# Kernel tuning notes

Hardware: AMD Instinct MI355X
Metric: run time of the kernel (lower is better)

The kernel has to match this reference:

```python
import jax, jax.numpy as jnp
import numpy as np

B, F, H = 16384, 2048, 4096   # batch, n_features, n_hidden
D, K = 4096, 2048             # num_of_demos, num_of_features


def setup_inputs() -> dict:
    key = jax.random.key(0)
    ks = jax.random.split(key, 16)
    s = 0.02
    return {
        "x": jax.random.normal(ks[0], (B, F), jnp.float32),
        "demo_metric": jax.random.uniform(ks[1], (D, K), jnp.float32),
        "alpha": jax.random.normal(ks[2], (K,), jnp.float32),
        "sample_loss": jax.random.uniform(ks[3], (D, K), jnp.float32),
        "subdom_constant": jax.random.uniform(ks[4], (1,), jnp.float32),
        "num_of_demos": D,
        "num_of_features": K,
        "W1": jax.random.normal(ks[5], (F, H), jnp.float32) * s,
        "b1": jnp.zeros((H,), jnp.float32),
        "W2": jax.random.normal(ks[6], (H, H), jnp.float32) * s,
        "b2": jnp.zeros((H,), jnp.float32),
        "W3": jax.random.normal(ks[7], (H, H), jnp.float32) * s,
        "b3": jnp.zeros((H,), jnp.float32),
        "W4": jax.random.normal(ks[8], (H, 2), jnp.float32) * s,
        "b4": jnp.zeros((2,), jnp.float32),
    }


def reference(x, demo_metric, alpha, sample_loss, subdom_constant,
              num_of_demos, num_of_features,
              W1, b1, W2, b2, W3, b3, W4, b4):
    # subdom hinge loss: max(alpha_k * (sample_loss_jk - demo_loss_jk) + 1, 0) - c
    margin = alpha[None, :] * (sample_loss - demo_metric) + 1.0  # [D, K]
    subdom = jnp.maximum(margin, 0.0) - subdom_constant          # broadcast c
    loss = jnp.sum(subdom)

    # MLP classifier (dropout = identity at inference) + sigmoid
    h = jax.nn.relu(x @ W1 + b1)
    h = jax.nn.relu(h @ W2 + b2)
    h = jax.nn.relu(h @ W3 + b3)
    probs = jax.nn.sigmoid(h @ W4 + b4)  # [B, 2]
    return (loss, probs)
```

## Files before the change

### kernel.cpp

```cpp
#include <hip/hip_runtime.h>
#include <cstdint>
#include <cstddef>

typedef unsigned short u16;
typedef __attribute__((ext_vector_type(8))) __bf16 bf16x8;
typedef __attribute__((ext_vector_type(4))) float f32x4;

__device__ __forceinline__ u16 f2bf(float f) {
  union { float f; unsigned u; } v; v.f = f;
  unsigned r = v.u + 0x7FFFu + ((v.u >> 16) & 1u);
  return (u16)(r >> 16);
}
__device__ __forceinline__ float bf2f(unsigned h) {
  union { unsigned u; float f; } v; v.u = h << 16;
  return v.f;
}

__global__ void init_loss_kernel(const float* __restrict__ c,
                                 const int* __restrict__ D,
                                 const int* __restrict__ K,
                                 float* __restrict__ out) {
  out[0] = -c[0] * (float)D[0] * (float)K[0];
}

__global__ void subdom_kernel(const float4* __restrict__ dm,
                              const float4* __restrict__ sl,
                              const float4* __restrict__ alpha4,
                              float* __restrict__ out, int n4, int k4mask) {
  const int stride = gridDim.x * blockDim.x;
  float s = 0.f;
  for (int i = blockIdx.x * blockDim.x + threadIdx.x; i < n4; i += stride) {
    float4 d = dm[i], l = sl[i], a = alpha4[i & k4mask];
    s += fmaxf(fmaf(a.x, l.x - d.x, 1.f), 0.f);
    s += fmaxf(fmaf(a.y, l.y - d.y, 1.f), 0.f);
    s += fmaxf(fmaf(a.z, l.z - d.z, 1.f), 0.f);
    s += fmaxf(fmaf(a.w, l.w - d.w, 1.f), 0.f);
  }
#pragma unroll
  for (int off = 32; off > 0; off >>= 1) s += __shfl_down(s, off, 64);
  __shared__ float red[4];
  const int lane = threadIdx.x & 63, wave = threadIdx.x >> 6;
  if (lane == 0) red[wave] = s;
  __syncthreads();
  if (threadIdx.x == 0) atomicAdd(out, red[0] + red[1] + red[2] + red[3]);
}

__global__ void cast_f32_bf16_kernel(const float4* __restrict__ in,
                                     u16* __restrict__ out, int n4) {
  const int stride = gridDim.x * blockDim.x;
  for (int i = blockIdx.x * blockDim.x + threadIdx.x; i < n4; i += stride) {
    float4 v = in[i];
    uint2 p;
    p.x = (unsigned)f2bf(v.x) | ((unsigned)f2bf(v.y) << 16);
    p.y = (unsigned)f2bf(v.z) | ((unsigned)f2bf(v.w) << 16);
    ((uint2*)out)[i] = p;
  }
}

__global__ void transpose_cast_kernel(const float* __restrict__ in,
                                      u16* __restrict__ out, int K, int N) {
  __shared__ float tile[32][33];
  const int bx = blockIdx.x * 32;
  const int by = blockIdx.y * 32;
  const int tx = threadIdx.x, ty = threadIdx.y;
#pragma unroll
  for (int i = ty; i < 32; i += 8)
    tile[i][tx] = in[(size_t)(by + i) * N + bx + tx];
  __syncthreads();
#pragma unroll
  for (int i = ty; i < 32; i += 8)
    out[(size_t)(bx + i) * K + by + tx] = f2bf(tile[tx][i]);
}


__device__ __forceinline__ void gload_lds16(const void* g, void* l) {
  __builtin_amdgcn_global_load_lds(
      (const __attribute__((address_space(1))) void*)g,
      (__attribute__((address_space(3))) void*)l, 16, 0, 0);
}

#define VMW(N) asm volatile("s_waitcnt vmcnt(" #N ")" ::: "memory")
#define MF(a, b, c) __builtin_amdgcn_mfma_f32_16x16x32_bf16(a, b, c, 0, 0, 0)

#define STAGE_A(BU, Q, TK)                                                    \
  gload_lds16(A + aGbase + (size_t)((Q)*64) * K + (size_t)(TK)*64,            \
              (void*)(As + ((BU)*4 + (Q)) * 4096 + swave))

#define STAGE_B(BU, NH, HH, TK)                                               \
  gload_lds16(Bt + bGbase + (size_t)((NH)*32 + (HH)*128) * K +                \
                  (size_t)(TK)*64,                                            \
              (void*)(Bs + ((BU)*2 + (NH)) * 8192 + (HH)*4096 + swave))

#define PHASE(BUF, MH, NH, LA, LB, BF, STAGE_CODE, WAIT_CODE)                 \
  {                                                                           \
    if (LA) {                                                                 \
      const u16* Ar_ = As + ((BUF)*4 + (wm << 1) + (MH)) * 4096 + abase;      \
      _Pragma("unroll") for (int f_ = 0; f_ < 4; ++f_) {                      \
        af0[f_] = *(const bf16x8*)(Ar_ + f_ * 1024 + aslot0);                 \
        af1[f_] = *(const bf16x8*)(Ar_ + f_ * 1024 + aslot1);                 \
      }                                                                       \
    }                                                                         \
    if (LB) {                                                                 \
      const u16* Br_ = Bs + ((BUF)*2 + (NH)) * 8192 + bbase;                  \
      BF[0] = *(const bf16x8*)(Br_ + aslot0);                                 \
      BF[1] = *(const bf16x8*)(Br_ + aslot1);                                 \
      BF[2] = *(const bf16x8*)(Br_ + 1024 + aslot0);                          \
      BF[3] = *(const bf16x8*)(Br_ + 1024 + aslot1);                          \
    }                                                                         \
    STAGE_CODE;                                                               \
    __builtin_amdgcn_s_barrier();                                             \
    __builtin_amdgcn_s_setprio(1);                                            \
    _Pragma("unroll") for (int f_ = 0; f_ < 4; ++f_) {                        \
      acc[(MH)*4 + f_][(NH)*2 + 0] = MF(af0[f_], BF[0], acc[(MH)*4 + f_][(NH)*2 + 0]); \
      acc[(MH)*4 + f_][(NH)*2 + 0] = MF(af1[f_], BF[1], acc[(MH)*4 + f_][(NH)*2 + 0]); \
      acc[(MH)*4 + f_][(NH)*2 + 1] = MF(af0[f_], BF[2], acc[(MH)*4 + f_][(NH)*2 + 1]); \
      acc[(MH)*4 + f_][(NH)*2 + 1] = MF(af1[f_], BF[3], acc[(MH)*4 + f_][(NH)*2 + 1]); \
    }                                                                         \
    __builtin_amdgcn_s_setprio(0);                                            \
    WAIT_CODE;                                                                \
    __builtin_amdgcn_s_barrier();                                             \
  }

__global__ __launch_bounds__(512, 2) void gemm256(
    const u16* __restrict__ A, const u16* __restrict__ Bt,
    const float* __restrict__ bias, u16* __restrict__ C,
    int M, int N, int K, int act) {
  __shared__ __align__(16) u16 As[2 * 4 * 4096];
  __shared__ __align__(16) u16 Bs[2 * 2 * 8192];

  const int gx = gridDim.x;
  const int bid = blockIdx.x + blockIdx.y * gx;
  const int cpx = (gx * gridDim.y) >> 3;
  const int tilei = (bid & 7) * cpx + (bid >> 3);
  const int m0 = (tilei / gx) * 256;
  const int n0 = (tilei % gx) * 256;

  const int tid = threadIdx.x;
  const int wave = tid >> 6, lane = tid & 63;
  const int l15 = lane & 15, quad = lane >> 4;
  const int wm = wave >> 2, wn = wave & 3;
  const int lsw = l15 & 7;

  const int aslot0 = ((quad ^ lsw) << 3);
  const int aslot1 = (((4 + quad) ^ lsw) << 3);
  const int abase = l15 * 64;
  const int bbase = (wn * 32 + l15) * 64;

  const int srow = tid >> 3;
  const int skch = ((tid & 7) ^ (srow & 7)) << 3;
  const int brow = ((srow >> 5) << 6) + (srow & 31);
  const size_t aGbase = (size_t)(m0 + srow) * K + skch;
  const size_t bGbase = (size_t)(n0 + brow) * K + skch;
  const int swave = wave * 512;

  f32x4 acc[8][4];
#pragma unroll
  for (int i = 0; i < 8; ++i)
#pragma unroll
    for (int j = 0; j < 4; ++j) acc[i][j] = (f32x4){0.f, 0.f, 0.f, 0.f};
  bf16x8 af0[4], af1[4], bfr0[4], bfr1[4];

  STAGE_A(0, 0, 0); STAGE_A(0, 1, 0); STAGE_A(0, 2, 0); STAGE_A(0, 3, 0);
  STAGE_B(0, 0, 0, 0); STAGE_B(0, 0, 1, 0);
  STAGE_B(0, 1, 0, 0); STAGE_B(0, 1, 1, 0);
  STAGE_A(1, 0, 1); STAGE_A(1, 2, 1);
  VMW(2);
  __builtin_amdgcn_s_barrier();

  const int niter = K >> 7;
  for (int it = 0; it < niter; ++it) {
    const int t1 = 2 * it + 1, t2 = 2 * it + 2, t3 = 2 * it + 3;
    const bool nl = (it + 1 < niter);
    PHASE(0, 0, 0, 1, 1, bfr0,
          { STAGE_B(1, 0, 0, t1); STAGE_B(1, 0, 1, t1); }, { VMW(6); });
    PHASE(0, 0, 1, 0, 1, bfr1,
          { STAGE_B(1, 1, 0, t1); STAGE_B(1, 1, 1, t1); }, { VMW(4); });
    PHASE(0, 1, 0, 1, 0, bfr0,
          { if (nl) { STAGE_A(0, 0, t2); STAGE_A(0, 2, t2); } }, {});
    PHASE(0, 1, 1, 0, 0, bfr1,
          { STAGE_A(1, 1, t1); STAGE_A(1, 3, t1); },
          { if (nl) { VMW(6); } else { VMW(4); } });
    PHASE(1, 0, 0, 1, 1, bfr0,
          { if (nl) { STAGE_B(0, 0, 0, t2); STAGE_B(0, 0, 1, t2); } },
          { if (nl) { VMW(6); } else { VMW(2); } });
    PHASE(1, 0, 1, 0, 1, bfr1,
          { if (nl) { STAGE_B(0, 1, 0, t2); STAGE_B(0, 1, 1, t2); } },
          { if (nl) { VMW(4); } else { VMW(0); } });
    PHASE(1, 1, 0, 1, 0, bfr0,
          { if (nl) { STAGE_A(1, 0, t3); STAGE_A(1, 2, t3); } }, {});
    PHASE(1, 1, 1, 0, 0, bfr1,
          { if (nl) { STAGE_A(0, 1, t2); STAGE_A(0, 3, t2); } },
          { if (nl) { VMW(6); } });
  }

#pragma unroll
  for (int mi = 0; mi < 8; ++mi) {
    const int row = m0 + wm * 128 + (mi >> 2) * 64 + (mi & 3) * 16 + quad * 4;
#pragma unroll
    for (int j = 0; j < 4; ++j) {
      const int col = n0 + wn * 64 + j * 16 + l15;
      const float bv = bias[col];
#pragma unroll
      for (int r = 0; r < 4; ++r) {
        float v = acc[mi][j][r] + bv;
        if (act) v = fmaxf(v, 0.f);
        C[(size_t)(row + r) * N + col] = f2bf(v);
      }
    }
  }
}

__global__ __launch_bounds__(256) void head_kernel(
    const u16* __restrict__ h, const float2* __restrict__ W4,
    const float* __restrict__ b4, float* __restrict__ out, int H) {
  const int row = blockIdx.x;
  const u16* hr = h + (size_t)row * H;
  const int tid = threadIdx.x;
  float p0 = 0.f, p1 = 0.f;
#pragma unroll
  for (int ii = 0; ii < 2; ++ii) {
    const int base = tid * 16 + ii * 8;
    const uint4 hv = *(const uint4*)(hr + base);
    const unsigned uu[4] = {hv.x, hv.y, hv.z, hv.w};
#pragma unroll
    for (int j = 0; j < 4; ++j) {
      float a0 = bf2f(uu[j] & 0xffffu);
      float a1 = bf2f(uu[j] >> 16);
      float2 w0 = W4[base + 2 * j];
      float2 w1 = W4[base + 2 * j + 1];
      p0 += a0 * w0.x + a1 * w1.x;
      p1 += a0 * w0.y + a1 * w1.y;
    }
  }
#pragma unroll
  for (int off = 32; off > 0; off >>= 1) {
    p0 += __shfl_down(p0, off, 64);
    p1 += __shfl_down(p1, off, 64);
  }
  __shared__ float r0[4], r1[4];
  const int lane = tid & 63, wave = tid >> 6;
  if (lane == 0) { r0[wave] = p0; r1[wave] = p1; }
  __syncthreads();
  if (tid == 0) {
    float l0 = r0[0] + r0[1] + r0[2] + r0[3] + b4[0];
    float l1 = r1[0] + r1[1] + r1[2] + r1[3] + b4[1];
    out[1 + row * 2] = 1.f / (1.f + __expf(-l0));
    out[2 + row * 2] = 1.f / (1.f + __expf(-l1));
  }
}

extern "C" void kernel_launch(void* const* d_in, const int* in_sizes, int n_in,
                              void* d_out, int out_size, void* d_ws,
                              size_t ws_size, hipStream_t stream) {
  (void)in_sizes; (void)n_in; (void)out_size; (void)ws_size;
  const float* x  = (const float*)d_in[0];
  const float* dm = (const float*)d_in[1];
  const float* al = (const float*)d_in[2];
  const float* sl = (const float*)d_in[3];
  const float* sc = (const float*)d_in[4];
  const int*   nd = (const int*)d_in[5];
  const int*   nf = (const int*)d_in[6];
  const float* W1 = (const float*)d_in[7];
  const float* b1 = (const float*)d_in[8];
  const float* W2 = (const float*)d_in[9];
  const float* b2 = (const float*)d_in[10];
  const float* W3 = (const float*)d_in[11];
  const float* b3 = (const float*)d_in[12];
  const float* W4 = (const float*)d_in[13];
  const float* b4 = (const float*)d_in[14];
  float* out = (float*)d_out;

  const int B = 16384, F = 2048, H = 4096, D = 4096, K = 2048;

  char* ws = (char*)d_ws;
  u16* xb = (u16*)ws;
  u16* wt = (u16*)(ws + (size_t)B * F * 2);
  u16* hA = (u16*)(ws + (size_t)B * F * 2 + (size_t)H * H * 2);
  u16* hB = hA + (size_t)B * H;

  init_loss_kernel<<<1, 1, 0, stream>>>(sc, nd, nf, out);
  subdom_kernel<<<1024, 256, 0, stream>>>((const float4*)dm, (const float4*)sl,
                                          (const float4*)al, out, D * K / 4,
                                          K / 4 - 1);
  cast_f32_bf16_kernel<<<4096, 256, 0, stream>>>((const float4*)x, xb, B * F / 4);
  transpose_cast_kernel<<<dim3(H / 32, F / 32), dim3(32, 8), 0, stream>>>(W1, wt, F, H);
  gemm256<<<dim3(H / 256, B / 256), 512, 0, stream>>>(xb, wt, b1, hA, B, H, F, 1);
  transpose_cast_kernel<<<dim3(H / 32, H / 32), dim3(32, 8), 0, stream>>>(W2, wt, H, H);
  gemm256<<<dim3(H / 256, B / 256), 512, 0, stream>>>(hA, wt, b2, hB, B, H, H, 1);
  transpose_cast_kernel<<<dim3(H / 32, H / 32), dim3(32, 8), 0, stream>>>(W3, wt, H, H);
  gemm256<<<dim3(H / 256, B / 256), 512, 0, stream>>>(hB, wt, b3, hA, B, H, H, 1);
  head_kernel<<<B, 256, 0, stream>>>(hA, (const float2*)W4, b4, out, H);
}
```

Baseline: 1.812 ms.

## Prefetch B fragments one phase early and drop mid-phase barrier in GEMM loop

Restructures the GEMM main loop so B-fragment LDS reads are issued one phase ahead (BRD in the preceding phase) and removes the barrier between staging and MFMA in each phase. The last iteration is peeled into an epilogue so the loop body needs no conditional staging or waits. This is meant to hide LDS read latency and cut barrier count. In exchange it changes the wait-count schedule, which risks LDS read/write hazards if the counts are wrong.

Measured after the change: 1.691 ms. -6.7%, faster.

```diff
diff --git a/kernel.cpp b/kernel.cpp
--- a/kernel.cpp
+++ b/kernel.cpp
@@ -91,7 +91,16 @@
                   (size_t)(TK)*64,                                            \
               (void*)(Bs + ((BU)*2 + (NH)) * 8192 + (HH)*4096 + swave))
 
-#define PHASE(BUF, MH, NH, LA, LB, BF, STAGE_CODE, WAIT_CODE)                 \
+#define BRD(BF, BU, NH2)                                                      \
+  {                                                                           \
+    const u16* Br_ = Bs + ((BU)*2 + (NH2)) * 8192 + bbase;                    \
+    BF[0] = *(const bf16x8*)(Br_ + aslot0);                                   \
+    BF[1] = *(const bf16x8*)(Br_ + aslot1);                                   \
+    BF[2] = *(const bf16x8*)(Br_ + 1024 + aslot0);                            \
+    BF[3] = *(const bf16x8*)(Br_ + 1024 + aslot1);                            \
+  }
+
+#define PH(BUF, MH, NH, LA, BF, PRE_CODE, STAGE_CODE, WAIT_CODE)              \
   {                                                                           \
     if (LA) {                                                                 \
       const u16* Ar_ = As + ((BUF)*4 + (wm << 1) + (MH)) * 4096 + abase;      \
@@ -100,15 +109,8 @@
         af1[f_] = *(const bf16x8*)(Ar_ + f_ * 1024 + aslot1);                 \
       }                                                                       \
     }                                                                         \
-    if (LB) {                                                                 \
-      const u16* Br_ = Bs + ((BUF)*2 + (NH)) * 8192 + bbase;                  \
-      BF[0] = *(const bf16x8*)(Br_ + aslot0);                                 \
-      BF[1] = *(const bf16x8*)(Br_ + aslot1);                                 \
-      BF[2] = *(const bf16x8*)(Br_ + 1024 + aslot0);                          \
-      BF[3] = *(const bf16x8*)(Br_ + 1024 + aslot1);                          \
-    }                                                                         \
+    PRE_CODE;                                                                 \
     STAGE_CODE;                                                               \
-    __builtin_amdgcn_s_barrier();                                             \
     __builtin_amdgcn_s_setprio(1);                                            \
     _Pragma("unroll") for (int f_ = 0; f_ < 4; ++f_) {                        \
       acc[(MH)*4 + f_][(NH)*2 + 0] = MF(af0[f_], BF[0], acc[(MH)*4 + f_][(NH)*2 + 0]); \
@@ -166,31 +168,41 @@
   STAGE_A(1, 0, 1); STAGE_A(1, 2, 1);
   VMW(2);
   __builtin_amdgcn_s_barrier();
+  BRD(bfr0, 0, 0);
 
   const int niter = K >> 7;
-  for (int it = 0; it < niter; ++it) {
+  for (int it = 0; it < niter - 1; ++it) {
     const int t1 = 2 * it + 1, t2 = 2 * it + 2, t3 = 2 * it + 3;
-    const bool nl = (it + 1 < niter);
-    PHASE(0, 0, 0, 1, 1, bfr0,
-          { STAGE_B(1, 0, 0, t1); STAGE_B(1, 0, 1, t1); }, { VMW(6); });
-    PHASE(0, 0, 1, 0, 1, bfr1,
-          { STAGE_B(1, 1, 0, t1); STAGE_B(1, 1, 1, t1); }, { VMW(4); });
-    PHASE(0, 1, 0, 1, 0, bfr0,
-          { if (nl) { STAGE_A(0, 0, t2); STAGE_A(0, 2, t2); } }, {});
-    PHASE(0, 1, 1, 0, 0, bfr1,
-          { STAGE_A(1, 1, t1); STAGE_A(1, 3, t1); },
-          { if (nl) { VMW(6); } else { VMW(4); } });
-    PHASE(1, 0, 0, 1, 1, bfr0,
-          { if (nl) { STAGE_B(0, 0, 0, t2); STAGE_B(0, 0, 1, t2); } },
-          { if (nl) { VMW(6); } else { VMW(2); } });
-    PHASE(1, 0, 1, 0, 1, bfr1,
-          { if (nl) { STAGE_B(0, 1, 0, t2); STAGE_B(0, 1, 1, t2); } },
-          { if (nl) { VMW(4); } else { VMW(0); } });
-    PHASE(1, 1, 0, 1, 0, bfr0,
-          { if (nl) { STAGE_A(1, 0, t3); STAGE_A(1, 2, t3); } }, {});
-    PHASE(1, 1, 1, 0, 0, bfr1,
-          { if (nl) { STAGE_A(0, 1, t2); STAGE_A(0, 3, t2); } },
-          { if (nl) { VMW(6); } });
+    PH(0, 0, 0, 1, bfr0, {},
+       { STAGE_B(1, 0, 0, t1); STAGE_B(1, 0, 1, t1); }, { VMW(6); });
+    PH(0, 0, 1, 0, bfr1, BRD(bfr1, 0, 1),
+       { STAGE_B(1, 1, 0, t1); STAGE_B(1, 1, 1, t1); }, { VMW(4); });
+    PH(0, 1, 0, 1, bfr0, {},
+       { STAGE_A(0, 0, t2); STAGE_A(0, 2, t2); }, { VMW(4); });
+    PH(0, 1, 1, 0, bfr1, BRD(bfr0, 1, 0),
+       { STAGE_A(1, 1, t1); STAGE_A(1, 3, t1); }, {});
+    PH(1, 0, 0, 1, bfr0, {},
+       { STAGE_B(0, 0, 0, t2); STAGE_B(0, 0, 1, t2); }, { VMW(6); });
+    PH(1, 0, 1, 0, bfr1, BRD(bfr1, 1, 1),
+       { STAGE_B(0, 1, 0, t2); STAGE_B(0, 1, 1, t2); }, { VMW(4); });
+    PH(1, 1, 0, 1, bfr0, {},
+       { STAGE_A(1, 0, t3); STAGE_A(1, 2, t3); }, { VMW(4); });
+    PH(1, 1, 1, 0, bfr1, BRD(bfr0, 0, 0),
+       { STAGE_A(0, 1, t2); STAGE_A(0, 3, t2); }, {});
+  }
+  {
+    const int t1 = 2 * niter - 1;
+    PH(0, 0, 0, 1, bfr0, {},
+       { STAGE_B(1, 0, 0, t1); STAGE_B(1, 0, 1, t1); }, { VMW(6); });
+    PH(0, 0, 1, 0, bfr1, BRD(bfr1, 0, 1),
+       { STAGE_B(1, 1, 0, t1); STAGE_B(1, 1, 1, t1); }, { VMW(4); });
+    PH(0, 1, 0, 1, bfr0, {}, {}, { VMW(2); });
+    PH(0, 1, 1, 0, bfr1, BRD(bfr0, 1, 0),
+       { STAGE_A(1, 1, t1); STAGE_A(1, 3, t1); }, {});
+    PH(1, 0, 0, 1, bfr0, {}, {}, { VMW(2); });
+    PH(1, 0, 1, 0, bfr1, BRD(bfr1, 1, 1), {}, { VMW(0); });
+    PH(1, 1, 0, 1, bfr0, {}, {}, {});
+    PH(1, 1, 1, 0, bfr1, {}, {}, {});
   }
 
 #pragma unroll
```
